# Performance work log

Measured on AMD Instinct MI355X. Metric: run time of the kernel, lower is better.

The kernel has to match this reference:

```python
import jax, jax.numpy as jnp
import numpy as np

EPS = 1e-6
STEPS = 6  # eval_steps == train_steps == 6


def _l2norm(v, axis, eps=1e-12):
    # F.normalize: v / max(||v||, eps)
    return v / jnp.maximum(jnp.linalg.norm(v, axis=axis, keepdims=True), eps)


def _conv1x1(x, w, b=None):
    # x: [B,C,H,W], w: [O,C]
    y = jnp.einsum('bchw,oc->bohw', x, w)
    if b is not None:
        y = y + b[None, :, None, None]
    return y


def _nmf_local_inference(x, bases):
    # x: [B,D,N], bases: [B,D,R]; torch.no_grad loop
    coef = jax.nn.softmax(jnp.einsum('bdn,bdr->bnr', x, bases), axis=-1)  # inv_t = 1

    def step(carry, _):
        bases, coef = carry
        # coef update
        xtb = jnp.einsum('bdn,bdr->bnr', x, bases)
        btb = jnp.einsum('bdr,bds->brs', bases, bases)
        coef = coef * xtb / (jnp.einsum('bnr,brs->bns', coef, btb) + EPS)
        # bases update
        xc = jnp.einsum('bdn,bnr->bdr', x, coef)
        ctc = jnp.einsum('bnr,bns->brs', coef, coef)
        bases = bases * xc / (jnp.einsum('bdr,brs->bds', bases, ctc) + EPS)
        return (bases, coef), None

    (bases, coef), _ = jax.lax.scan(step, (bases, coef), None, length=STEPS)
    return bases, coef


def _nmf_compute_coef(x, bases, coef):
    # differentiable final coef refinement
    xtb = jnp.einsum('bdn,bdr->bnr', x, bases)
    btb = jnp.einsum('bdr,bds->brs', bases, bases)
    return coef * xtb / (jnp.einsum('bnr,brs->bns', coef, btb) + EPS)


def _ham_nmf(h, bases0):
    # h: [B,C,H,W], S=1 -> D=C, N=H*W
    B, C, H, W = h.shape
    x = h.reshape(B, C, H * W)
    sg = jax.lax.stop_gradient
    bases, coef = _nmf_local_inference(sg(x), bases0)
    bases, coef = sg(bases), sg(coef)
    coef = _nmf_compute_coef(x, bases, coef)
    out = jnp.einsum('bdr,bnr->bdn', bases, coef)  # bases @ coef^T
    return out.reshape(B, C, H, W)


def reference(x, bases0, w_lower, b_lower, w_cheese, b_cheese, w_upper,
              coef_shortcut, coef_ham):
    shortcut = x
    # lower bread: 1x1 conv + ReLU (NMF variant)
    h = jax.nn.relu(_conv1x1(x, w_lower, b_lower))
    # hamburger (NMF2D, spatial=True, rand_init bases normalized over D)
    bases = _l2norm(bases0, axis=1)
    h = _ham_nmf(h, bases)
    # cheese: 1x1 conv + ReLU (norm_cfg=None -> conv has bias)
    h = jax.nn.relu(_conv1x1(h, w_cheese, b_cheese))
    # upper bread: 1x1 conv, no bias
    h = _conv1x1(h, w_upper)
    return jax.nn.relu(coef_ham * h + coef_shortcut * shortcut)


def setup_inputs() -> dict:
    key = jax.random.key(0)
    ks = jax.random.split(key, 8)
    B, in_c, Hh, Ww = 8, 512, 64, 64
    C, R = 512, 64
    std = (2.0 / C) ** 0.5  # kaiming-style init from _init_weight (1x1 convs)
    std_up = (2.0 / in_c) ** 0.5
    return {
        'x': jax.random.normal(ks[0], (B, in_c, Hh, Ww), jnp.float32),
        'bases0': jax.random.uniform(ks[1], (B, C, R), jnp.float32),
        'w_lower': jax.random.normal(ks[2], (C, in_c), jnp.float32) * std,
        'b_lower': jnp.zeros((C,), jnp.float32),
        'w_cheese': jax.random.normal(ks[3], (C, C), jnp.float32) * std,
        'b_cheese': jnp.zeros((C,), jnp.float32),
        'w_upper': jax.random.normal(ks[4], (in_c, C), jnp.float32) * std_up,
        'coef_shortcut': jnp.ones((1,), jnp.float32),
        'coef_ham': jnp.ones((1,), jnp.float32),
    }
```

## Files before the change

### kernel.cpp

```cpp
#include <hip/hip_runtime.h>

#define NMF_EPS 1e-6f

typedef unsigned short ushort_t;
typedef __attribute__((ext_vector_type(8))) short bf16x8;
typedef __attribute__((ext_vector_type(4))) float f32x4;

__device__ __forceinline__ ushort_t f2bf(float f) {
    unsigned int u = __float_as_uint(f);
    return (ushort_t)((u + 0x7FFFu + ((u >> 16) & 1u)) >> 16);
}
__device__ __forceinline__ float bf2f(ushort_t h) {
    return __uint_as_float(((unsigned int)h) << 16);
}

__device__ __forceinline__ void gl_lds16(const ushort_t* g, ushort_t* l) {
    __builtin_amdgcn_global_load_lds(
        (const __attribute__((address_space(1))) unsigned int*)g,
        (__attribute__((address_space(3))) unsigned int*)l,
        16, 0, 0);
}

template<int SPLIT, int EPI>
__global__ __launch_bounds__(256) void mfma_gemm(
    const ushort_t* __restrict__ Ah, const ushort_t* __restrict__ Al,
    const ushort_t* __restrict__ Bh, const ushort_t* __restrict__ Bl,
    float* __restrict__ C, ushort_t* __restrict__ Chi, ushort_t* __restrict__ Clo,
    int M, int N, int K,
    long sB, long sC,
    const float* __restrict__ bias,
    const float* __restrict__ res, long sRes,
    const float* __restrict__ hamp, const float* __restrict__ scp)
{
    __shared__ char smem[SPLIT ? 32768 : 16384];
    ushort_t* sAh = (ushort_t*)smem;
    ushort_t* sBh = (ushort_t*)(smem + 8192);
    ushort_t* sAl = SPLIT ? (ushort_t*)(smem + 16384) : nullptr;
    ushort_t* sBl = SPLIT ? (ushort_t*)(smem + 24576) : nullptr;

    const int tid  = threadIdx.x;
    const int wave = tid >> 6, lane = tid & 63;
    const int quad = lane >> 4, lr = lane & 15;
    const int batch = blockIdx.z;
    const int m0 = blockIdx.y * 128, n0 = blockIdx.x * 128;

    const ushort_t* Bhb = Bh + (long)batch * sB;
    const ushort_t* Blb = SPLIT ? (Bl + (long)batch * sB) : nullptr;

    f32x4 acc[4][4];
    #pragma unroll
    for (int i = 0; i < 4; ++i)
        #pragma unroll
        for (int j = 0; j < 4; ++j)
            acc[i][j] = (f32x4){0.f, 0.f, 0.f, 0.f};

    const int q   = wave * 2;
    const int ra0 = (q + 0) * 16 + (lane >> 2);
    const int ra1 = (q + 1) * 16 + (lane >> 2);
    const int ko  = (lane & 3) * 8;
    const int wm = (wave & 1) * 64, wn = (wave >> 1) * 64;

    for (int k0 = 0; k0 < K; k0 += 32) {
        gl_lds16(&Ah [(long)(m0 + ra0) * K + k0 + ko], &sAh[(q + 0) * 512]);
        gl_lds16(&Ah [(long)(m0 + ra1) * K + k0 + ko], &sAh[(q + 1) * 512]);
        gl_lds16(&Bhb[(long)(n0 + ra0) * K + k0 + ko], &sBh[(q + 0) * 512]);
        gl_lds16(&Bhb[(long)(n0 + ra1) * K + k0 + ko], &sBh[(q + 1) * 512]);
        if constexpr (SPLIT) {
            gl_lds16(&Al [(long)(m0 + ra0) * K + k0 + ko], &sAl[(q + 0) * 512]);
            gl_lds16(&Al [(long)(m0 + ra1) * K + k0 + ko], &sAl[(q + 1) * 512]);
            gl_lds16(&Blb[(long)(n0 + ra0) * K + k0 + ko], &sBl[(q + 0) * 512]);
            gl_lds16(&Blb[(long)(n0 + ra1) * K + k0 + ko], &sBl[(q + 1) * 512]);
        }
        __syncthreads();

        bf16x8 af[4], bfr[4], afl[4], bfl[4];
        #pragma unroll
        for (int i = 0; i < 4; ++i)
            af[i] = *(const bf16x8*)&sAh[(wm + i * 16 + lr) * 32 + quad * 8];
        #pragma unroll
        for (int j = 0; j < 4; ++j)
            bfr[j] = *(const bf16x8*)&sBh[(wn + j * 16 + lr) * 32 + quad * 8];
        if constexpr (SPLIT) {
            #pragma unroll
            for (int i = 0; i < 4; ++i)
                afl[i] = *(const bf16x8*)&sAl[(wm + i * 16 + lr) * 32 + quad * 8];
            #pragma unroll
            for (int j = 0; j < 4; ++j)
                bfl[j] = *(const bf16x8*)&sBl[(wn + j * 16 + lr) * 32 + quad * 8];
        }

        #pragma unroll
        for (int i = 0; i < 4; ++i)
            #pragma unroll
            for (int j = 0; j < 4; ++j) {
                acc[i][j] = __builtin_amdgcn_mfma_f32_16x16x32_bf16(af[i], bfr[j], acc[i][j], 0, 0, 0);
                if constexpr (SPLIT) {
                    acc[i][j] = __builtin_amdgcn_mfma_f32_16x16x32_bf16(af[i], bfl[j], acc[i][j], 0, 0, 0);
                    acc[i][j] = __builtin_amdgcn_mfma_f32_16x16x32_bf16(afl[i], bfr[j], acc[i][j], 0, 0, 0);
                }
            }
        __syncthreads();
    }

    if (EPI == 2) {
        ushort_t* Hh = Chi + (long)batch * sC;
        ushort_t* Hl = Clo + (long)batch * sC;
        unsigned int* slab = (unsigned int*)smem;
        #pragma unroll
        for (int p = 0; p < 2; ++p) {
            __syncthreads();
            if ((wave & 1) == p) {
                #pragma unroll
                for (int i = 0; i < 4; ++i) {
                    const int mb = m0 + p * 64 + i * 16 + quad * 4;
                    #pragma unroll
                    for (int j = 0; j < 4; ++j) {
                        const int nl = wn + j * 16 + lr;
                        #pragma unroll
                        for (int r = 0; r < 4; ++r) {
                            float v = fmaxf(acc[i][j][r] + bias[mb + r], 0.f);
                            ushort_t h = f2bf(v);
                            ushort_t l = f2bf(v - bf2f(h));
                            slab[nl * 64 + (i * 16 + quad * 4 + r)] =
                                (unsigned)h | ((unsigned)l << 16);
                        }
                    }
                }
            }
            __syncthreads();
            for (int idx = tid; idx < 8192; idx += 256) {
                const int nl = idx >> 6, ml = idx & 63;
                unsigned u = slab[idx];
                const long off = (long)(n0 + nl) * M + m0 + p * 64 + ml;
                Hh[off] = (ushort_t)(u & 0xffffu);
                Hl[off] = (ushort_t)(u >> 16);
            }
        }
    } else {
        const float hm = *hamp, sc = *scp;
        float* Cb = C + (long)batch * sC;
        #pragma unroll
        for (int i = 0; i < 4; ++i) {
            #pragma unroll
            for (int j = 0; j < 4; ++j) {
                const int mbase = m0 + wm + i * 16 + quad * 4;
                const int n     = n0 + wn + j * 16 + lr;
                #pragma unroll
                for (int r = 0; r < 4; ++r) {
                    float rv = res[(long)batch * sRes + (long)(mbase + r) * N + n];
                    Cb[(long)(mbase + r) * N + n] = fmaxf(fmaf(hm, acc[i][j][r], sc * rv), 0.f);
                }
            }
        }
    }
}

template<int MODE>
__global__ __launch_bounds__(256) void coef_step(
    const ushort_t* __restrict__ Xh, const ushort_t* __restrict__ Xl,
    const ushort_t* __restrict__ bth, const ushort_t* __restrict__ btl,
    const float* __restrict__ btb_part,
    float* __restrict__ coef,
    ushort_t* __restrict__ cth, ushort_t* __restrict__ ctl,
    float* __restrict__ ctc_part,
    int Bcnt)
{
    __shared__ char smem[32768 + 18432];
    ushort_t* stg = (ushort_t*)smem;
    ushort_t* gLh = (ushort_t*)(smem + 32768);
    ushort_t* gLl = gLh + 64 * 72;

    const int tid = threadIdx.x, wave = tid >> 6, lane = tid & 63;
    const int quad = lane >> 4, lr = lane & 15;
    const int b = blockIdx.y, n0 = blockIdx.x * 64;

    const ushort_t* Xhb  = Xh  + (long)b * 2097152 + (long)n0 * 512;
    const ushort_t* Xlb  = Xl  + (long)b * 2097152 + (long)n0 * 512;
    const ushort_t* bthb = bth + (long)b * 32768;
    const ushort_t* btlb = btl + (long)b * 32768;
    float* coefB = coef + (long)b * 262144 + (long)n0 * 64;

    if (MODE == 1) {
        for (int i = tid; i < 4096; i += 256) {
            const int r = i >> 6, s = i & 63;
            float v = 0.f;
            #pragma unroll
            for (int c = 0; c < 8; ++c)
                v += btb_part[((long)c * Bcnt + b) * 4096 + i];
            ushort_t h = f2bf(v);
            gLh[r * 72 + s] = h;
            gLl[r * 72 + s] = f2bf(v - bf2f(h));
        }
    }

    const int srow = wave * 16 + (lane >> 2);
    const int koff = (lane & 3) * 8;
    f32x4 accx[4];
    #pragma unroll
    for (int j = 0; j < 4; ++j) accx[j] = (f32x4){0.f, 0.f, 0.f, 0.f};

    for (int kt = 0; kt < 512; kt += 64) {
        #pragma unroll
        for (int kc = 0; kc < 2; ++kc) {
            const int kg = kt + kc * 32 + koff;
            gl_lds16(&Xhb [(long)srow * 512 + kg], &stg[(0 * 2 + kc) * 2048 + wave * 512]);
            gl_lds16(&Xlb [(long)srow * 512 + kg], &stg[(1 * 2 + kc) * 2048 + wave * 512]);
            gl_lds16(&bthb[(long)srow * 512 + kg], &stg[(2 * 2 + kc) * 2048 + wave * 512]);
            gl_lds16(&btlb[(long)srow * 512 + kg], &stg[(3 * 2 + kc) * 2048 + wave * 512]);
        }
        __syncthreads();
        #pragma unroll
        for (int kc = 0; kc < 2; ++kc) {
            bf16x8 ah = *(const bf16x8*)&stg[(0 * 2 + kc) * 2048 + (wave * 16 + lr) * 32 + quad * 8];
            bf16x8 al = *(const bf16x8*)&stg[(1 * 2 + kc) * 2048 + (wave * 16 + lr) * 32 + quad * 8];
            #pragma unroll
            for (int j = 0; j < 4; ++j) {
                bf16x8 bh = *(const bf16x8*)&stg[(2 * 2 + kc) * 2048 + (j * 16 + lr) * 32 + quad * 8];
                bf16x8 bl = *(const bf16x8*)&stg[(3 * 2 + kc) * 2048 + (j * 16 + lr) * 32 + quad * 8];
                accx[j] = __builtin_amdgcn_mfma_f32_16x16x32_bf16(ah, bh, accx[j], 0, 0, 0);
                accx[j] = __builtin_amdgcn_mfma_f32_16x16x32_bf16(ah, bl, accx[j], 0, 0, 0);
                accx[j] = __builtin_amdgcn_mfma_f32_16x16x32_bf16(al, bh, accx[j], 0, 0, 0);
            }
        }
        __syncthreads();
    }

    float cnew[4][4];
    if (MODE == 1) {
        f32x4 accd[4];
        #pragma unroll
        for (int j = 0; j < 4; ++j) accd[j] = (f32x4){0.f, 0.f, 0.f, 0.f};
        #pragma unroll
        for (int kk = 0; kk < 2; ++kk) {
            const float* cp = &coefB[(wave * 16 + lr) * 64 + kk * 32 + quad * 8];
            float4 cA = *(const float4*)cp;
            float4 cB = *(const float4*)(cp + 4);
            float cv[8] = {cA.x, cA.y, cA.z, cA.w, cB.x, cB.y, cB.z, cB.w};
            bf16x8 ah, al;
            #pragma unroll
            for (int e = 0; e < 8; ++e) {
                ushort_t h = f2bf(cv[e]);
                ((short*)&ah)[e] = (short)h;
                ((short*)&al)[e] = (short)f2bf(cv[e] - bf2f(h));
            }
            #pragma unroll
            for (int j = 0; j < 4; ++j) {
                bf16x8 bh = *(const bf16x8*)&gLh[(j * 16 + lr) * 72 + kk * 32 + quad * 8];
                bf16x8 bl = *(const bf16x8*)&gLl[(j * 16 + lr) * 72 + kk * 32 + quad * 8];
                accd[j] = __builtin_amdgcn_mfma_f32_16x16x32_bf16(ah, bh, accd[j], 0, 0, 0);
                accd[j] = __builtin_amdgcn_mfma_f32_16x16x32_bf16(ah, bl, accd[j], 0, 0, 0);
                accd[j] = __builtin_amdgcn_mfma_f32_16x16x32_bf16(al, bh, accd[j], 0, 0, 0);
            }
        }
        #pragma unroll
        for (int j = 0; j < 4; ++j)
            #pragma unroll
            for (int r = 0; r < 4; ++r) {
                float cold = coefB[(wave * 16 + quad * 4 + r) * 64 + j * 16 + lr];
                cnew[j][r] = cold * accx[j][r] / (accd[j][r] + NMF_EPS);
            }
    } else {
        #pragma unroll
        for (int r = 0; r < 4; ++r) {
            float m = fmaxf(fmaxf(accx[0][r], accx[1][r]), fmaxf(accx[2][r], accx[3][r]));
            #pragma unroll
            for (int off = 1; off < 16; off <<= 1) m = fmaxf(m, __shfl_xor(m, off, 64));
            float e[4], s = 0.f;
            #pragma unroll
            for (int j = 0; j < 4; ++j) { e[j] = __expf(accx[j][r] - m); s += e[j]; }
            #pragma unroll
            for (int off = 1; off < 16; off <<= 1) s += __shfl_xor(s, off, 64);
            float inv = 1.f / s;
            #pragma unroll
            for (int j = 0; j < 4; ++j) cnew[j][r] = e[j] * inv;
        }
    }

    #pragma unroll
    for (int j = 0; j < 4; ++j)
        #pragma unroll
        for (int r = 0; r < 4; ++r)
            coefB[(wave * 16 + quad * 4 + r) * 64 + j * 16 + lr] = cnew[j][r];

    if (MODE == 0) return;

    __syncthreads();
    #pragma unroll
    for (int j = 0; j < 4; ++j)
        #pragma unroll
        for (int r = 0; r < 4; ++r) {
            const int nl = wave * 16 + quad * 4 + r;
            const int rr = j * 16 + lr;
            float v = cnew[j][r];
            ushort_t h = f2bf(v);
            gLh[rr * 72 + nl] = h;
            gLl[rr * 72 + nl] = f2bf(v - bf2f(h));
        }
    __syncthreads();
    for (int i = tid; i < 4096; i += 256) {
        const int r = i >> 6, nn = i & 63;
        cth[(long)b * 262144 + (long)r * 4096 + n0 + nn] = gLh[r * 72 + nn];
        ctl[(long)b * 262144 + (long)r * 4096 + n0 + nn] = gLl[r * 72 + nn];
    }
    f32x4 accc[4];
    #pragma unroll
    for (int j = 0; j < 4; ++j) accc[j] = (f32x4){0.f, 0.f, 0.f, 0.f};
    #pragma unroll
    for (int kk = 0; kk < 64; kk += 32) {
        bf16x8 ah = *(const bf16x8*)&gLh[(wave * 16 + lr) * 72 + kk + quad * 8];
        bf16x8 al = *(const bf16x8*)&gLl[(wave * 16 + lr) * 72 + kk + quad * 8];
        #pragma unroll
        for (int j = 0; j < 4; ++j) {
            bf16x8 bh = *(const bf16x8*)&gLh[(j * 16 + lr) * 72 + kk + quad * 8];
            bf16x8 bl = *(const bf16x8*)&gLl[(j * 16 + lr) * 72 + kk + quad * 8];
            accc[j] = __builtin_amdgcn_mfma_f32_16x16x32_bf16(ah, bh, accc[j], 0, 0, 0);
            accc[j] = __builtin_amdgcn_mfma_f32_16x16x32_bf16(ah, bl, accc[j], 0, 0, 0);
            accc[j] = __builtin_amdgcn_mfma_f32_16x16x32_bf16(al, bh, accc[j], 0, 0, 0);
        }
    }
    float* cp = ctc_part + ((long)blockIdx.x * Bcnt + b) * 4096;
    #pragma unroll
    for (int j = 0; j < 4; ++j)
        #pragma unroll
        for (int r = 0; r < 4; ++r)
            cp[(wave * 16 + quad * 4 + r) * 64 + j * 16 + lr] = accc[j][r];
}

__global__ __launch_bounds__(256) void ctc_reduce(const float* __restrict__ part,
                                                  float* __restrict__ ctc, int Bcnt)
{
    const int b = blockIdx.x >> 4;
    const int i = (blockIdx.x & 15) * 256 + threadIdx.x;
    float v = 0.f;
    #pragma unroll 8
    for (int c = 0; c < 64; ++c)
        v += part[((long)c * Bcnt + b) * 4096 + i];
    ctc[(long)b * 4096 + i] = v;
}

__global__ __launch_bounds__(256) void xc_partial(
    const ushort_t* __restrict__ Ah, const ushort_t* __restrict__ Al,
    const ushort_t* __restrict__ Bh, const ushort_t* __restrict__ Bl,
    float* __restrict__ part, int Bcnt)
{
    __shared__ ushort_t stg[8 * 2048];
    const int tid = threadIdx.x, wave = tid >> 6, lane = tid & 63;
    const int quad = lane >> 4, lr = lane & 15;
    const int batch = blockIdx.z;
    const int m0 = blockIdx.y * 64;
    const int k0 = blockIdx.x * 512;

    const ushort_t* Ab  = Ah + (long)batch * 2097152;
    const ushort_t* Alb = Al + (long)batch * 2097152;
    const ushort_t* Bb  = Bh + (long)batch * 262144;
    const ushort_t* Blb = Bl + (long)batch * 262144;

    const int srow = wave * 16 + (lane >> 2);
    const int koff = (lane & 3) * 8;

    f32x4 acc[4];
    #pragma unroll
    for (int j = 0; j < 4; ++j) acc[j] = (f32x4){0.f, 0.f, 0.f, 0.f};

    for (int kt = 0; kt < 512; kt += 64) {
        #pragma unroll
        for (int kc = 0; kc < 2; ++kc) {
            const int kg = k0 + kt + kc * 32 + koff;
            gl_lds16(&Ab [(long)(m0 + srow) * 4096 + kg], &stg[(0 * 2 + kc) * 2048 + wave * 512]);
            gl_lds16(&Alb[(long)(m0 + srow) * 4096 + kg], &stg[(1 * 2 + kc) * 2048 + wave * 512]);
            gl_lds16(&Bb [(long)srow * 4096 + kg], &stg[(2 * 2 + kc) * 2048 + wave * 512]);
            gl_lds16(&Blb[(long)srow * 4096 + kg], &stg[(3 * 2 + kc) * 2048 + wave * 512]);
        }
        __syncthreads();
        #pragma unroll
        for (int kc = 0; kc < 2; ++kc) {
            bf16x8 ah = *(const bf16x8*)&stg[(0 * 2 + kc) * 2048 + (wave * 16 + lr) * 32 + quad * 8];
            bf16x8 al = *(const bf16x8*)&stg[(1 * 2 + kc) * 2048 + (wave * 16 + lr) * 32 + quad * 8];
            #pragma unroll
            for (int j = 0; j < 4; ++j) {
                bf16x8 bh = *(const bf16x8*)&stg[(2 * 2 + kc) * 2048 + (j * 16 + lr) * 32 + quad * 8];
                bf16x8 bl = *(const bf16x8*)&stg[(3 * 2 + kc) * 2048 + (j * 16 + lr) * 32 + quad * 8];
                acc[j] = __builtin_amdgcn_mfma_f32_16x16x32_bf16(ah, bh, acc[j], 0, 0, 0);
                acc[j] = __builtin_amdgcn_mfma_f32_16x16x32_bf16(ah, bl, acc[j], 0, 0, 0);
                acc[j] = __builtin_amdgcn_mfma_f32_16x16x32_bf16(al, bh, acc[j], 0, 0, 0);
            }
        }
        __syncthreads();
    }

    float* Cb = part + ((long)blockIdx.x * Bcnt + batch) * 32768;
    #pragma unroll
    for (int j = 0; j < 4; ++j) {
        const int col = j * 16 + lr;
        #pragma unroll
        for (int r = 0; r < 4; ++r)
            Cb[(long)(m0 + wave * 16 + quad * 4 + r) * 64 + col] = acc[j][r];
    }
}

template<int MODE>
__global__ __launch_bounds__(256) void bases_step(
    const float* __restrict__ xc_part,
    const float* __restrict__ ctc,
    float* __restrict__ bases,
    ushort_t* __restrict__ bth, ushort_t* __restrict__ btl,
    float* __restrict__ btb_part,
    int Bcnt)
{
    __shared__ char smem[16640 * 2 + 18432];
    float* bnL  = (float*)smem;
    float* ctcL = (float*)(smem + 16640);
    ushort_t* btLh = (ushort_t*)(smem + 33280);
    ushort_t* btLl = btLh + 64 * 72;
    float* basesL = (float*)(smem + 33280);

    const int b = blockIdx.y, c0 = blockIdx.x * 64;
    const int tid = threadIdx.x;
    float* basesB = bases + (long)b * 32768 + (long)c0 * 64;

    if (MODE == 1) {
        for (int i = tid; i < 4096; i += 256) {
            const int c = i >> 6, r = i & 63;
            basesL[c * 65 + r] = basesB[i];
            ctcL[c * 65 + r]   = ctc[(long)b * 4096 + i];
            float v = 0.f;
            #pragma unroll
            for (int s0 = 0; s0 < 8; ++s0)
                v += xc_part[((long)s0 * Bcnt + b) * 32768 + (long)(c0 + c) * 64 + r];
            bnL[c * 65 + r] = v;
        }
        __syncthreads();
        for (int i = tid; i < 4096; i += 256) {
            const int c = i >> 6, r = i & 63;
            float denom = 0.f;
            #pragma unroll 8
            for (int s = 0; s < 64; ++s)
                denom = fmaf(basesL[c * 65 + s], ctcL[s * 65 + r], denom);
            float bnew = basesL[c * 65 + r] * bnL[c * 65 + r] / (denom + NMF_EPS);
            bnL[c * 65 + r] = bnew;
            basesB[i] = bnew;
        }
        __syncthreads();
    } else {
        for (int i = tid; i < 4096; i += 256)
            bnL[(i >> 6) * 65 + (i & 63)] = basesB[i];
        __syncthreads();
    }

    for (int i = tid; i < 4096; i += 256) {
        const int r = i >> 6, cc = i & 63;
        float v = bnL[cc * 65 + r];
        ushort_t h = f2bf(v);
        ushort_t l = f2bf(v - bf2f(h));
        btLh[r * 72 + cc] = h;
        btLl[r * 72 + cc] = l;
        bth[(long)b * 32768 + (long)r * 512 + c0 + cc] = h;
        btl[(long)b * 32768 + (long)r * 512 + c0 + cc] = l;
    }
    __syncthreads();

    const int wave = tid >> 6, lane = tid & 63;
    const int quad = lane >> 4, lr = lane & 15;
    f32x4 acg[4];
    #pragma unroll
    for (int j = 0; j < 4; ++j) acg[j] = (f32x4){0.f, 0.f, 0.f, 0.f};
    #pragma unroll
    for (int kk = 0; kk < 64; kk += 32) {
        bf16x8 ah = *(const bf16x8*)&btLh[(wave * 16 + lr) * 72 + kk + quad * 8];
        bf16x8 al = *(const bf16x8*)&btLl[(wave * 16 + lr) * 72 + kk + quad * 8];
        #pragma unroll
        for (int j = 0; j < 4; ++j) {
            bf16x8 bh = *(const bf16x8*)&btLh[(j * 16 + lr) * 72 + kk + quad * 8];
            bf16x8 bl = *(const bf16x8*)&btLl[(j * 16 + lr) * 72 + kk + quad * 8];
            acg[j] = __builtin_amdgcn_mfma_f32_16x16x32_bf16(ah, bh, acg[j], 0, 0, 0);
            acg[j] = __builtin_amdgcn_mfma_f32_16x16x32_bf16(ah, bl, acg[j], 0, 0, 0);
            acg[j] = __builtin_amdgcn_mfma_f32_16x16x32_bf16(al, bh, acg[j], 0, 0, 0);
        }
    }
    float* gp = btb_part + ((long)blockIdx.x * Bcnt + b) * 4096;
    #pragma unroll
    for (int j = 0; j < 4; ++j)
        #pragma unroll
        for (int r = 0; r < 4; ++r)
            gp[(wave * 16 + quad * 4 + r) * 64 + j * 16 + lr] = acg[j][r];
}

constexpr int BM = 64, BN = 64, BK = 16;

template<int ALAY, int BLAY, int EPI>
__global__ __launch_bounds__(256) void gemm_kernel(
    const float* __restrict__ A, const float* __restrict__ B, float* __restrict__ C,
    int Kchunk, int kchunks,
    int lda, int ldb, int ldc,
    long sA, long sB, long sC,
    const float* __restrict__ bias)
{
    __shared__ float As[BK][BM + 4];
    __shared__ float Bs[BK][BN + 4];

    const int batch = blockIdx.z;
    const float* Ab = A + (long)batch * sA;
    const float* Bb = B + (long)batch * sB;

    const int m0  = blockIdx.y * BM;
    const int n0  = blockIdx.x * BN;
    const int tid = threadIdx.x;
    const int ty  = tid >> 4, tx = tid & 15;

    float acc[4][4] = {};

    for (int kt = 0; kt < Kchunk; kt += BK) {
        if (ALAY == 0) {
            const int m = tid >> 2, k4 = (tid & 3) << 2;
            float4 v = *(const float4*)&Ab[(long)(m0 + m) * lda + (kt + k4)];
            As[k4 + 0][m] = v.x; As[k4 + 1][m] = v.y;
            As[k4 + 2][m] = v.z; As[k4 + 3][m] = v.w;
        } else {
            const int k = tid >> 4, m4 = (tid & 15) << 2;
            float4 v = *(const float4*)&Ab[(long)(kt + k) * lda + (m0 + m4)];
            *(float4*)&As[k][m4] = v;
        }
        if (BLAY == 0) {
            const int k = tid >> 4, n4 = (tid & 15) << 2;
            float4 v = *(const float4*)&Bb[(long)(kt + k) * ldb + (n0 + n4)];
            *(float4*)&Bs[k][n4] = v;
        } else {
            const int n = tid >> 2, k4 = (tid & 3) << 2;
            float4 v = *(const float4*)&Bb[(long)(n0 + n) * ldb + (kt + k4)];
            Bs[k4 + 0][n] = v.x; Bs[k4 + 1][n] = v.y;
            Bs[k4 + 2][n] = v.z; Bs[k4 + 3][n] = v.w;
        }
        __syncthreads();
        #pragma unroll
        for (int k = 0; k < BK; ++k) {
            float4 a4 = *(const float4*)&As[k][ty << 2];
            float4 b4 = *(const float4*)&Bs[k][tx << 2];
            float av[4] = {a4.x, a4.y, a4.z, a4.w};
            float bv[4] = {b4.x, b4.y, b4.z, b4.w};
            #pragma unroll
            for (int i = 0; i < 4; ++i)
                #pragma unroll
                for (int j = 0; j < 4; ++j)
                    acc[i][j] = fmaf(av[i], bv[j], acc[i][j]);
        }
        __syncthreads();
    }

    const int mb = m0 + (ty << 2), nb = n0 + (tx << 2);
    if (EPI == 4) {
        ushort_t* Cu = (ushort_t*)C + (long)batch * sC;
        #pragma unroll
        for (int j = 0; j < 4; ++j) {
            ushort_t pk[4];
            #pragma unroll
            for (int i = 0; i < 4; ++i)
                pk[i] = f2bf(fmaxf(acc[i][j] + bias[mb + i], 0.f));
            *(ushort4*)&Cu[(long)(nb + j) * ldc + mb] =
                make_ushort4(pk[0], pk[1], pk[2], pk[3]);
        }
    } else {
        float* Cb = C + (long)batch * sC;
        #pragma unroll
        for (int i = 0; i < 4; ++i) {
            float4 o = make_float4(acc[i][0], acc[i][1], acc[i][2], acc[i][3]);
            *(float4*)&Cb[(long)(mb + i) * ldc + nb] = o;
        }
    }
}

__global__ __launch_bounds__(256) void cast_x_t(const float* __restrict__ x,
                                                ushort_t* __restrict__ hi,
                                                ushort_t* __restrict__ lo)
{
    __shared__ float t[64][65];
    const int b = blockIdx.z, c0 = blockIdx.y * 64, n0 = blockIdx.x * 64;
    const int tid = threadIdx.x, tx = tid & 63, ty = tid >> 6;
    const float* xb = x + (long)b * 512 * 4096;
    #pragma unroll 4
    for (int s = ty; s < 64; s += 4)
        t[s][tx] = xb[(long)(c0 + s) * 4096 + n0 + tx];
    __syncthreads();
    #pragma unroll 4
    for (int s = ty; s < 64; s += 4) {
        float v = t[tx][s];
        long idx = (long)b * 2097152 + (long)(n0 + s) * 512 + c0 + tx;
        ushort_t h = f2bf(v);
        hi[idx] = h;
        lo[idx] = f2bf(v - bf2f(h));
    }
}

__global__ __launch_bounds__(256) void nd2dn(const ushort_t* __restrict__ hi,
                                             const ushort_t* __restrict__ lo,
                                             ushort_t* __restrict__ dhi,
                                             ushort_t* __restrict__ dlo)
{
    __shared__ unsigned int t[64][65];
    const int b = blockIdx.z, n0 = blockIdx.x * 64, c0 = blockIdx.y * 64;
    const int tx = threadIdx.x & 63, ty = threadIdx.x >> 6;
    const long base = (long)b * 2097152;
    #pragma unroll 4
    for (int s = ty; s < 64; s += 4) {
        long idx = base + (long)(n0 + s) * 512 + c0 + tx;
        t[s][tx] = (unsigned)hi[idx] | ((unsigned)lo[idx] << 16);
    }
    __syncthreads();
    #pragma unroll 4
    for (int s = ty; s < 64; s += 4) {
        unsigned v = t[tx][s];
        long idx = base + (long)(c0 + s) * 4096 + n0 + tx;
        dhi[idx] = (ushort_t)(v & 0xffffu);
        dlo[idx] = (ushort_t)(v >> 16);
    }
}

__global__ void cast_w_split(const float* __restrict__ w, ushort_t* __restrict__ hi,
                             ushort_t* __restrict__ lo, int n)
{
    int i = blockIdx.x * 256 + threadIdx.x;
    if (i < n) {
        float v = w[i];
        ushort_t h = f2bf(v);
        hi[i] = h;
        lo[i] = f2bf(v - bf2f(h));
    }
}

__global__ void cast_w_plain(const float* __restrict__ w, ushort_t* __restrict__ o, int n)
{
    int i = blockIdx.x * 256 + threadIdx.x;
    if (i < n) o[i] = f2bf(w[i]);
}

__global__ __launch_bounds__(1024) void l2norm_kernel(const float* __restrict__ b0,
                                                      float* __restrict__ bases)
{
    __shared__ float part[16][64];
    const int b = blockIdx.x;
    const int tid = threadIdx.x;
    const int r = tid & 63, slice = tid >> 6;
    const float* src = b0 + (long)b * 512 * 64;
    float* dst = bases + (long)b * 512 * 64;
    float s = 0.f;
    #pragma unroll 4
    for (int d = slice; d < 512; d += 16) {
        float v = src[d * 64 + r];
        s = fmaf(v, v, s);
    }
    part[slice][r] = s;
    __syncthreads();
    if (slice == 0) {
        float t = 0.f;
        #pragma unroll
        for (int i = 0; i < 16; ++i) t += part[i][r];
        part[0][r] = 1.0f / fmaxf(sqrtf(t), 1e-12f);
    }
    __syncthreads();
    const float inv = part[0][r];
    #pragma unroll 4
    for (int d = slice; d < 512; d += 16)
        dst[d * 64 + r] = src[d * 64 + r] * inv;
}

extern "C" void kernel_launch(void* const* d_in, const int* in_sizes, int n_in,
                              void* d_out, int out_size, void* d_ws, size_t ws_size,
                              hipStream_t stream)
{
    const float* x_in     = (const float*)d_in[0];
    const float* bases0   = (const float*)d_in[1];
    const float* w_lower  = (const float*)d_in[2];
    const float* b_lower  = (const float*)d_in[3];
    const float* w_cheese = (const float*)d_in[4];
    const float* b_cheese = (const float*)d_in[5];
    const float* w_upper  = (const float*)d_in[6];
    const float* csc      = (const float*)d_in[7];
    const float* cham     = (const float*)d_in[8];
    float* out = (float*)d_out;

    const int B = 8, C = 512, N = 4096, R = 64;
    const long sCN = (long)C * N;
    const long sNC = (long)N * C;
    const long sNR = (long)N * R, sCR = (long)C * R;

    char* w = (char*)d_ws;
    ushort_t* X_nd_hi  = (ushort_t*)w;  w += 33554432;
    ushort_t* xt_hi    = (ushort_t*)w;  w += 33554432;
    ushort_t* xt_lo    = (ushort_t*)w;  w += 33554432;
    float*    coef     = (float*)w;     w += 8388608;
    ushort_t* ct_hi    = (ushort_t*)w;  w += 4194304;
    ushort_t* ct_lo    = (ushort_t*)w;  w += 4194304;
    float*    ctc_part = (float*)w;     w += 8388608;
    float*    xc_part  = (float*)w;     w += 8388608;
    float*    btb_part = (float*)w;     w += 1048576;
    float*    bases    = (float*)w;     w += 1048576;
    float*    WcB      = (float*)w;     w += 1048576;
    float*    ctc      = (float*)w;     w += 131072;
    ushort_t* bt_hi    = (ushort_t*)w;  w += 524288;
    ushort_t* bt_lo    = (ushort_t*)w;  w += 524288;
    ushort_t* wl_hi    = (ushort_t*)w;  w += 524288;
    ushort_t* wl_lo    = (ushort_t*)w;  w += 524288;
    ushort_t* w_up     = (ushort_t*)w;  w += 524288;

    ushort_t* X_nd_lo;
    {
        const size_t used = (size_t)(w - (char*)d_ws);
        if (ws_size >= used + 33554432UL) {
            X_nd_lo = (ushort_t*)w;  w += 33554432;
        } else {
            X_nd_lo = (ushort_t*)d_out;
        }
    }

    ushort_t* X_dn_hi  = xt_hi;
    ushort_t* X_dn_lo  = xt_lo;
    ushort_t* cheese_t = X_nd_hi;

    const dim3 blk(256);

    l2norm_kernel<<<dim3(B), dim3(1024), 0, stream>>>(bases0, bases);
    bases_step<0><<<dim3(C / 64, B), blk, 0, stream>>>(
        nullptr, nullptr, bases, bt_hi, bt_lo, btb_part, B);
    cast_w_split<<<dim3(1024), blk, 0, stream>>>(w_lower, wl_hi, wl_lo, C * C);
    cast_w_plain<<<dim3(1024), blk, 0, stream>>>(w_upper, w_up, C * C);
    cast_x_t<<<dim3(N / 64, C / 64, B), blk, 0, stream>>>(x_in, xt_hi, xt_lo);

    mfma_gemm<1, 2><<<dim3(N / 128, C / 128, B), blk, 0, stream>>>(
        wl_hi, wl_lo, xt_hi, xt_lo, nullptr, X_nd_hi, X_nd_lo,
        C, N, C, sNC, sNC, b_lower, nullptr, 0L, nullptr, nullptr);
    nd2dn<<<dim3(N / 64, C / 64, B), blk, 0, stream>>>(X_nd_hi, X_nd_lo, X_dn_hi, X_dn_lo);

    coef_step<0><<<dim3(N / 64, B), blk, 0, stream>>>(
        X_nd_hi, X_nd_lo, bt_hi, bt_lo, btb_part, coef, ct_hi, ct_lo, ctc_part, B);

    for (int step = 0; step < 6; ++step) {
        coef_step<1><<<dim3(N / 64, B), blk, 0, stream>>>(
            X_nd_hi, X_nd_lo, bt_hi, bt_lo, btb_part, coef, ct_hi, ct_lo, ctc_part, B);
        ctc_reduce<<<dim3(B * 16), blk, 0, stream>>>(ctc_part, ctc, B);
        xc_partial<<<dim3(8, C / 64, B), blk, 0, stream>>>(
            X_dn_hi, X_dn_lo, ct_hi, ct_lo, xc_part, B);
        bases_step<1><<<dim3(C / 64, B), blk, 0, stream>>>(
            xc_part, ctc, bases, bt_hi, bt_lo, btb_part, B);
    }

    coef_step<1><<<dim3(N / 64, B), blk, 0, stream>>>(
        X_nd_hi, X_nd_lo, bt_hi, bt_lo, btb_part, coef, ct_hi, ct_lo, ctc_part, B);

    gemm_kernel<0, 0, 0><<<dim3(1, C / BM, B), blk, 0, stream>>>(
        w_cheese, bases, WcB, C, 1, C, R, R, 0L, sCR, sCR, nullptr);
    gemm_kernel<0, 1, 4><<<dim3(N / BN, C / BM, B), blk, 0, stream>>>(
        WcB, coef, (float*)cheese_t, R, 1, R, R, C, sCR, sNR, sNC, b_cheese);

    mfma_gemm<0, 3><<<dim3(N / 128, C / 128, B), blk, 0, stream>>>(
        w_up, nullptr, cheese_t, nullptr, out, nullptr, nullptr,
        C, N, C, sNC, sCN, nullptr, x_in, sCN, cham, csc);
}
```

Baseline: 753.7 us.

## Double-buffer LDS staging, read small operands from global, fuse ctc reduction

Adds double-buffered LDS staging to the MFMA GEMM, coef_step and xc_partial kernels, so the next K tile is fetched while the current one is computed. In coef_step and xc_partial the small B operand (bases or coef tiles) is now read straight from global/L2 instead of being staged in LDS. The separate ctc_reduce kernel is removed and its reduction folded into bases_step, saving a launch per iteration. A new MODE 2 lets the final coef_step skip the unused ctc partial computation. The trade-offs are doubled LDS use, which may lower occupancy, redundant ctc reduction work in every bases_step block, and uncached global reads in inner loops.

```diff
diff --git a/kernel.cpp b/kernel.cpp
--- a/kernel.cpp
+++ b/kernel.cpp
@@ -32,11 +32,8 @@
     const float* __restrict__ res, long sRes,
     const float* __restrict__ hamp, const float* __restrict__ scp)
 {
-    __shared__ char smem[SPLIT ? 32768 : 16384];
-    ushort_t* sAh = (ushort_t*)smem;
-    ushort_t* sBh = (ushort_t*)(smem + 8192);
-    ushort_t* sAl = SPLIT ? (ushort_t*)(smem + 16384) : nullptr;
-    ushort_t* sBl = SPLIT ? (ushort_t*)(smem + 24576) : nullptr;
+    constexpr int SB = SPLIT ? 32768 : 16384;
+    __shared__ char smem[2 * SB];
 
     const int tid  = threadIdx.x;
     const int wave = tid >> 6, lane = tid & 63;
@@ -60,18 +57,34 @@
     const int ko  = (lane & 3) * 8;
     const int wm = (wave & 1) * 64, wn = (wave >> 1) * 64;
 
+    auto STAGE = [&](int buf, int k0) {
+        char* base = smem + buf * SB;
+        ushort_t* dAh = (ushort_t*)base;
+        ushort_t* dBh = (ushort_t*)(base + 8192);
+        gl_lds16(&Ah [(long)(m0 + ra0) * K + k0 + ko], &dAh[(q + 0) * 512]);
+        gl_lds16(&Ah [(long)(m0 + ra1) * K + k0 + ko], &dAh[(q + 1) * 512]);
+        gl_lds16(&Bhb[(long)(n0 + ra0) * K + k0 + ko], &dBh[(q + 0) * 512]);
+        gl_lds16(&Bhb[(long)(n0 + ra1) * K + k0 + ko], &dBh[(q + 1) * 512]);
+        if constexpr (SPLIT) {
+            ushort_t* dAl = (ushort_t*)(base + 16384);
+            ushort_t* dBl = (ushort_t*)(base + 24576);
+            gl_lds16(&Al [(long)(m0 + ra0) * K + k0 + ko], &dAl[(q + 0) * 512]);
+            gl_lds16(&Al [(long)(m0 + ra1) * K + k0 + ko], &dAl[(q + 1) * 512]);
+            gl_lds16(&Blb[(long)(n0 + ra0) * K + k0 + ko], &dBl[(q + 0) * 512]);
+            gl_lds16(&Blb[(long)(n0 + ra1) * K + k0 + ko], &dBl[(q + 1) * 512]);
+        }
+    };
+
+    STAGE(0, 0);
+    __syncthreads();
+    int cur = 0;
+
     for (int k0 = 0; k0 < K; k0 += 32) {
-        gl_lds16(&Ah [(long)(m0 + ra0) * K + k0 + ko], &sAh[(q + 0) * 512]);
-        gl_lds16(&Ah [(long)(m0 + ra1) * K + k0 + ko], &sAh[(q + 1) * 512]);
-        gl_lds16(&Bhb[(long)(n0 + ra0) * K + k0 + ko], &sBh[(q + 0) * 512]);
-        gl_lds16(&Bhb[(long)(n0 + ra1) * K + k0 + ko], &sBh[(q + 1) * 512]);
-        if constexpr (SPLIT) {
-            gl_lds16(&Al [(long)(m0 + ra0) * K + k0 + ko], &sAl[(q + 0) * 512]);
-            gl_lds16(&Al [(long)(m0 + ra1) * K + k0 + ko], &sAl[(q + 1) * 512]);
-            gl_lds16(&Blb[(long)(n0 + ra0) * K + k0 + ko], &sBl[(q + 0) * 512]);
-            gl_lds16(&Blb[(long)(n0 + ra1) * K + k0 + ko], &sBl[(q + 1) * 512]);
-        }
-        __syncthreads();
+        if (k0 + 32 < K) STAGE(cur ^ 1, k0 + 32);
+
+        char* base = smem + cur * SB;
+        ushort_t* sAh = (ushort_t*)base;
+        ushort_t* sBh = (ushort_t*)(base + 8192);
 
         bf16x8 af[4], bfr[4], afl[4], bfl[4];
         #pragma unroll
@@ -81,6 +94,8 @@
         for (int j = 0; j < 4; ++j)
             bfr[j] = *(const bf16x8*)&sBh[(wn + j * 16 + lr) * 32 + quad * 8];
         if constexpr (SPLIT) {
+            ushort_t* sAl = (ushort_t*)(base + 16384);
+            ushort_t* sBl = (ushort_t*)(base + 24576);
             #pragma unroll
             for (int i = 0; i < 4; ++i)
                 afl[i] = *(const bf16x8*)&sAl[(wm + i * 16 + lr) * 32 + quad * 8];
@@ -100,6 +115,7 @@
                 }
             }
         __syncthreads();
+        cur ^= 1;
     }
 
     if (EPI == 2) {
@@ -165,6 +181,7 @@
     float* __restrict__ ctc_part,
     int Bcnt)
 {
+    constexpr bool MU = (MODE >= 1);
     __shared__ char smem[32768 + 18432];
     ushort_t* stg = (ushort_t*)smem;
     ushort_t* gLh = (ushort_t*)(smem + 32768);
@@ -180,7 +197,7 @@
     const ushort_t* btlb = btl + (long)b * 32768;
     float* coefB = coef + (long)b * 262144 + (long)n0 * 64;
 
-    if (MODE == 1) {
+    if (MU) {
         for (int i = tid; i < 4096; i += 256) {
             const int r = i >> 6, s = i & 63;
             float v = 0.f;
@@ -199,34 +216,42 @@
     #pragma unroll
     for (int j = 0; j < 4; ++j) accx[j] = (f32x4){0.f, 0.f, 0.f, 0.f};
 
-    for (int kt = 0; kt < 512; kt += 64) {
+    auto STAGEX = [&](int buf, int kt) {
         #pragma unroll
         for (int kc = 0; kc < 2; ++kc) {
             const int kg = kt + kc * 32 + koff;
-            gl_lds16(&Xhb [(long)srow * 512 + kg], &stg[(0 * 2 + kc) * 2048 + wave * 512]);
-            gl_lds16(&Xlb [(long)srow * 512 + kg], &stg[(1 * 2 + kc) * 2048 + wave * 512]);
-            gl_lds16(&bthb[(long)srow * 512 + kg], &stg[(2 * 2 + kc) * 2048 + wave * 512]);
-            gl_lds16(&btlb[(long)srow * 512 + kg], &stg[(3 * 2 + kc) * 2048 + wave * 512]);
-        }
-        __syncthreads();
+            gl_lds16(&Xhb[(long)srow * 512 + kg], &stg[buf * 8192 + (0 * 2 + kc) * 2048 + wave * 512]);
+            gl_lds16(&Xlb[(long)srow * 512 + kg], &stg[buf * 8192 + (1 * 2 + kc) * 2048 + wave * 512]);
+        }
+    };
+
+    STAGEX(0, 0);
+    __syncthreads();
+    int cur = 0;
+
+    for (int kt = 0; kt < 512; kt += 64) {
+        if (kt + 64 < 512) STAGEX(cur ^ 1, kt + 64);
         #pragma unroll
         for (int kc = 0; kc < 2; ++kc) {
-            bf16x8 ah = *(const bf16x8*)&stg[(0 * 2 + kc) * 2048 + (wave * 16 + lr) * 32 + quad * 8];
-            bf16x8 al = *(const bf16x8*)&stg[(1 * 2 + kc) * 2048 + (wave * 16 + lr) * 32 + quad * 8];
+            bf16x8 ah = *(const bf16x8*)&stg[cur * 8192 + (0 * 2 + kc) * 2048 + (wave * 16 + lr) * 32 + quad * 8];
+            bf16x8 al = *(const bf16x8*)&stg[cur * 8192 + (1 * 2 + kc) * 2048 + (wave * 16 + lr) * 32 + quad * 8];
+            const int kg = kt + kc * 32 + quad * 8;
             #pragma unroll
             for (int j = 0; j < 4; ++j) {
-                bf16x8 bh = *(const bf16x8*)&stg[(2 * 2 + kc) * 2048 + (j * 16 + lr) * 32 + quad * 8];
-                bf16x8 bl = *(const bf16x8*)&stg[(3 * 2 + kc) * 2048 + (j * 16 + lr) * 32 + quad * 8];
+                const long boff = (long)(j * 16 + lr) * 512 + kg;
+                bf16x8 bh = *(const bf16x8*)&bthb[boff];
+                bf16x8 bl = *(const bf16x8*)&btlb[boff];
                 accx[j] = __builtin_amdgcn_mfma_f32_16x16x32_bf16(ah, bh, accx[j], 0, 0, 0);
                 accx[j] = __builtin_amdgcn_mfma_f32_16x16x32_bf16(ah, bl, accx[j], 0, 0, 0);
                 accx[j] = __builtin_amdgcn_mfma_f32_16x16x32_bf16(al, bh, accx[j], 0, 0, 0);
             }
         }
         __syncthreads();
+        cur ^= 1;
     }
 
     float cnew[4][4];
-    if (MODE == 1) {
+    if (MU) {
         f32x4 accd[4];
         #pragma unroll
         for (int j = 0; j < 4; ++j) accd[j] = (f32x4){0.f, 0.f, 0.f, 0.f};
@@ -282,7 +307,7 @@
         for (int r = 0; r < 4; ++r)
             coefB[(wave * 16 + quad * 4 + r) * 64 + j * 16 + lr] = cnew[j][r];
 
-    if (MODE == 0) return;
+    if (MODE != 1) return;
 
     __syncthreads();
     #pragma unroll
@@ -326,24 +351,12 @@
             cp[(wave * 16 + quad * 4 + r) * 64 + j * 16 + lr] = accc[j][r];
 }
 
-__global__ __launch_bounds__(256) void ctc_reduce(const float* __restrict__ part,
-                                                  float* __restrict__ ctc, int Bcnt)
-{
-    const int b = blockIdx.x >> 4;
-    const int i = (blockIdx.x & 15) * 256 + threadIdx.x;
-    float v = 0.f;
-    #pragma unroll 8
-    for (int c = 0; c < 64; ++c)
-        v += part[((long)c * Bcnt + b) * 4096 + i];
-    ctc[(long)b * 4096 + i] = v;
-}
-
 __global__ __launch_bounds__(256) void xc_partial(
     const ushort_t* __restrict__ Ah, const ushort_t* __restrict__ Al,
     const ushort_t* __restrict__ Bh, const ushort_t* __restrict__ Bl,
     float* __restrict__ part, int Bcnt)
 {
-    __shared__ ushort_t stg[8 * 2048];
+    __shared__ ushort_t stg[2 * 8192];
     const int tid = threadIdx.x, wave = tid >> 6, lane = tid & 63;
     const int quad = lane >> 4, lr = lane & 15;
     const int batch = blockIdx.z;
@@ -362,30 +375,38 @@
     #pragma unroll
     for (int j = 0; j < 4; ++j) acc[j] = (f32x4){0.f, 0.f, 0.f, 0.f};
 
-    for (int kt = 0; kt < 512; kt += 64) {
+    auto STAGEX = [&](int buf, int kt) {
         #pragma unroll
         for (int kc = 0; kc < 2; ++kc) {
             const int kg = k0 + kt + kc * 32 + koff;
-            gl_lds16(&Ab [(long)(m0 + srow) * 4096 + kg], &stg[(0 * 2 + kc) * 2048 + wave * 512]);
-            gl_lds16(&Alb[(long)(m0 + srow) * 4096 + kg], &stg[(1 * 2 + kc) * 2048 + wave * 512]);
-            gl_lds16(&Bb [(long)srow * 4096 + kg], &stg[(2 * 2 + kc) * 2048 + wave * 512]);
-            gl_lds16(&Blb[(long)srow * 4096 + kg], &stg[(3 * 2 + kc) * 2048 + wave * 512]);
-        }
-        __syncthreads();
+            gl_lds16(&Ab [(long)(m0 + srow) * 4096 + kg], &stg[buf * 8192 + (0 * 2 + kc) * 2048 + wave * 512]);
+            gl_lds16(&Alb[(long)(m0 + srow) * 4096 + kg], &stg[buf * 8192 + (1 * 2 + kc) * 2048 + wave * 512]);
+        }
+    };
+
+    STAGEX(0, 0);
+    __syncthreads();
+    int cur = 0;
+
+    for (int kt = 0; kt < 512; kt += 64) {
+        if (kt + 64 < 512) STAGEX(cur ^ 1, kt + 64);
         #pragma unroll
         for (int kc = 0; kc < 2; ++kc) {
-            bf16x8 ah = *(const bf16x8*)&stg[(0 * 2 + kc) * 2048 + (wave * 16 + lr) * 32 + quad * 8];
-            bf16x8 al = *(const bf16x8*)&stg[(1 * 2 + kc) * 2048 + (wave * 16 + lr) * 32 + quad * 8];
+            bf16x8 ah = *(const bf16x8*)&stg[cur * 8192 + (0 * 2 + kc) * 2048 + (wave * 16 + lr) * 32 + quad * 8];
+            bf16x8 al = *(const bf16x8*)&stg[cur * 8192 + (1 * 2 + kc) * 2048 + (wave * 16 + lr) * 32 + quad * 8];
+            const int kg = k0 + kt + kc * 32 + quad * 8;
             #pragma unroll
             for (int j = 0; j < 4; ++j) {
-                bf16x8 bh = *(const bf16x8*)&stg[(2 * 2 + kc) * 2048 + (j * 16 + lr) * 32 + quad * 8];
-                bf16x8 bl = *(const bf16x8*)&stg[(3 * 2 + kc) * 2048 + (j * 16 + lr) * 32 + quad * 8];
+                const long boff = (long)(j * 16 + lr) * 4096 + kg;
+                bf16x8 bh = *(const bf16x8*)&Bb [boff];
+                bf16x8 bl = *(const bf16x8*)&Blb[boff];
                 acc[j] = __builtin_amdgcn_mfma_f32_16x16x32_bf16(ah, bh, acc[j], 0, 0, 0);
                 acc[j] = __builtin_amdgcn_mfma_f32_16x16x32_bf16(ah, bl, acc[j], 0, 0, 0);
                 acc[j] = __builtin_amdgcn_mfma_f32_16x16x32_bf16(al, bh, acc[j], 0, 0, 0);
             }
         }
         __syncthreads();
+        cur ^= 1;
     }
 
     float* Cb = part + ((long)blockIdx.x * Bcnt + batch) * 32768;
@@ -401,7 +422,7 @@
 template<int MODE>
 __global__ __launch_bounds__(256) void bases_step(
     const float* __restrict__ xc_part,
-    const float* __restrict__ ctc,
+    const float* __restrict__ ctc_part,
     float* __restrict__ bases,
     ushort_t* __restrict__ bth, ushort_t* __restrict__ btl,
     float* __restrict__ btb_part,
@@ -422,7 +443,11 @@
         for (int i = tid; i < 4096; i += 256) {
             const int c = i >> 6, r = i & 63;
             basesL[c * 65 + r] = basesB[i];
-            ctcL[c * 65 + r]   = ctc[(long)b * 4096 + i];
+            float cv = 0.f;
+            #pragma unroll 8
+            for (int ch = 0; ch < 64; ++ch)
+                cv += ctc_part[((long)ch * Bcnt + b) * 4096 + i];
+            ctcL[c * 65 + r] = cv;
             float v = 0.f;
             #pragma unroll
             for (int s0 = 0; s0 < 8; ++s0)
@@ -694,7 +719,6 @@
     float*    btb_part = (float*)w;     w += 1048576;
     float*    bases    = (float*)w;     w += 1048576;
     float*    WcB      = (float*)w;     w += 1048576;
-    float*    ctc      = (float*)w;     w += 131072;
     ushort_t* bt_hi    = (ushort_t*)w;  w += 524288;
     ushort_t* bt_lo    = (ushort_t*)w;  w += 524288;
     ushort_t* wl_hi    = (ushort_t*)w;  w += 524288;
@@ -735,14 +759,13 @@
     for (int step = 0; step < 6; ++step) {
         coef_step<1><<<dim3(N / 64, B), blk, 0, stream>>>(
             X_nd_hi, X_nd_lo, bt_hi, bt_lo, btb_part, coef, ct_hi, ct_lo, ctc_part, B);
-        ctc_reduce<<<dim3(B * 16), blk, 0, stream>>>(ctc_part, ctc, B);
         xc_partial<<<dim3(8, C / 64, B), blk, 0, stream>>>(
             X_dn_hi, X_dn_lo, ct_hi, ct_lo, xc_part, B);
         bases_step<1><<<dim3(C / 64, B), blk, 0, stream>>>(
-            xc_part, ctc, bases, bt_hi, bt_lo, btb_part, B);
-    }
-
-    coef_step<1><<<dim3(N / 64, B), blk, 0, stream>>>(
+            xc_part, ctc_part, bases, bt_hi, bt_lo, btb_part, B);
+    }
+
+    coef_step<2><<<dim3(N / 64, B), blk, 0, stream>>>(
         X_nd_hi, X_nd_lo, bt_hi, bt_lo, btb_part, coef, ct_hi, ct_lo, ctc_part, B);
 
     gemm_kernel<0, 0, 0><<<dim3(1, C / BM, B), blk, 0, stream>>>(
```

Result: slower. 1.284 ms (+70.4%).
